# Kernel optimization log

Hardware: AMD Instinct MI355X
Metric: run time of the kernel (lower is better)

## Reference

```python
import jax, jax.numpy as jnp
import numpy as np

B, D, L = 32768, 1024, 4

def setup_inputs() -> dict:
    key = jax.random.key(0)
    k1, k2, k3 = jax.random.split(key, 3)
    x = jax.random.normal(k1, (B, D), dtype=jnp.float32)
    # torch init: normal_(0, 0.005) for both weights and biases, shape (d,1) -> flatten to (d,)
    weights = jax.random.normal(k2, (L, D), dtype=jnp.float32) * 0.005
    biases = jax.random.normal(k3, (L, D), dtype=jnp.float32) * 0.005
    return {"x": x, "weights": weights, "biases": biases}

def reference(x, weights, biases):
    # DCN cross layer: x_{i+1} = x0 * (x_i . w_i) + b_i + x_i
    # Algebraically identical to matmul(bmm(x0, x_i^T), w_i) + b_i + x_i
    x0 = x  # [B, D]

    def step(cur, wb):
        w, b = wb  # [D], [D]
        s = cur @ w  # [B] scalar per row (x_i^T w_i)
        cur = x0 * s[:, None] + b[None, :] + cur  # [B, D]
        return cur, None

    out, _ = jax.lax.scan(step, x, (weights, biases))
    return out  # [B, D] (squeeze of [B, D, 1])
```

## Files before the change

### kernel.cpp

```cpp
#include <hip/hip_runtime.h>


#define DCN_D 1024
#define DCN_F4 (DCN_D / 4)


__global__ __launch_bounds__(256) void dcn_pre_kernel(
    const float* __restrict__ w,
    const float* __restrict__ b,
    float* __restrict__ ws)
{
    const int t = threadIdx.x;
    for (int d = t; d < DCN_D; d += 256)
        ws[d] = b[d] + b[DCN_D + d] + b[2 * DCN_D + d] + b[3 * DCN_D + d];
    float p[6] = {0, 0, 0, 0, 0, 0};
    for (int d = t; d < DCN_D; d += 256) {
        const float b0 = b[d], b1 = b[DCN_D + d], b2 = b[2 * DCN_D + d];
        const float w1 = w[DCN_D + d], w2 = w[2 * DCN_D + d], w3 = w[3 * DCN_D + d];
        p[0] = fmaf(b0, w1, p[0]);
        p[1] = fmaf(b0, w2, p[1]);
        p[2] = fmaf(b1, w2, p[2]);
        p[3] = fmaf(b0, w3, p[3]);
        p[4] = fmaf(b1, w3, p[4]);
        p[5] = fmaf(b2, w3, p[5]);
    }
    __shared__ float red[6][4];
    const int wave = t >> 6, lane = t & 63;
    #pragma unroll
    for (int k = 0; k < 6; ++k) {
        float v = p[k];
        #pragma unroll
        for (int off = 32; off > 0; off >>= 1) v += __shfl_down(v, off, 64);
        if (lane == 0) red[k][wave] = v;
    }
    __syncthreads();
    if (t < 6) ws[DCN_D + t] = red[t][0] + red[t][1] + red[t][2] + red[t][3];
}

__device__ __forceinline__ void dcn_pair(
    const float4 xa[4], const float4 xb[4],
    const float4* __restrict__ w4, const float4 bv[4],
    float c01, float c2sum, float c3sum,
    float* __restrict__ out, int rowA, int rowB, int lane)
{
    float p0[4] = {0, 0, 0, 0}, p1[4] = {0, 0, 0, 0};
    #pragma unroll
    for (int j = 0; j < 4; ++j) {
        const int idx = lane + 64 * j;
        #pragma unroll
        for (int l = 0; l < 4; ++l) {
            const float4 wv = w4[l * DCN_F4 + idx];
            p0[l] = fmaf(xa[j].x, wv.x, fmaf(xa[j].y, wv.y,
                    fmaf(xa[j].z, wv.z, fmaf(xa[j].w, wv.w, p0[l]))));
            p1[l] = fmaf(xb[j].x, wv.x, fmaf(xb[j].y, wv.y,
                    fmaf(xb[j].z, wv.z, fmaf(xb[j].w, wv.w, p1[l]))));
        }
    }
    #pragma unroll
    for (int off = 1; off < 64; off <<= 1) {
        #pragma unroll
        for (int l = 0; l < 4; ++l) {
            p0[l] += __shfl_xor(p0[l], off, 64);
            p1[l] += __shfl_xor(p1[l], off, 64);
        }
    }
    const float t1a = 1.f + p0[0];
    const float s1a = fmaf(p0[1], t1a, c01);
    const float t2a = t1a + s1a;
    const float s2a = fmaf(p0[2], t2a, c2sum);
    const float t3a = t2a + s2a;
    const float s3a = fmaf(p0[3], t3a, c3sum);
    const float S0  = t3a + s3a;
    const float t1b = 1.f + p1[0];
    const float s1b = fmaf(p1[1], t1b, c01);
    const float t2b = t1b + s1b;
    const float s2b = fmaf(p1[2], t2b, c2sum);
    const float t3b = t2b + s2b;
    const float s3b = fmaf(p1[3], t3b, c3sum);
    const float S1  = t3b + s3b;

    float4* __restrict__ oA = reinterpret_cast<float4*>(out + (size_t)rowA * DCN_D);
    float4* __restrict__ oB = reinterpret_cast<float4*>(out + (size_t)rowB * DCN_D);
    #pragma unroll
    for (int j = 0; j < 4; ++j) {
        const int idx = lane + 64 * j;
        float4 a;
        a.x = fmaf(xa[j].x, S0, bv[j].x);
        a.y = fmaf(xa[j].y, S0, bv[j].y);
        a.z = fmaf(xa[j].z, S0, bv[j].z);
        a.w = fmaf(xa[j].w, S0, bv[j].w);
        oA[idx] = a;
        float4 c;
        c.x = fmaf(xb[j].x, S1, bv[j].x);
        c.y = fmaf(xb[j].y, S1, bv[j].y);
        c.z = fmaf(xb[j].z, S1, bv[j].z);
        c.w = fmaf(xb[j].w, S1, bv[j].w);
        oB[idx] = c;
    }
}

__global__ __launch_bounds__(256) void dcn_main_kernel(
    const float* __restrict__ x,
    const float* __restrict__ w,
    const float* __restrict__ ws,
    float* __restrict__ out,
    int B)
{
    const int wid  = (int)((blockIdx.x * 256u + threadIdx.x) >> 6);
    const int lane = (int)(threadIdx.x & 63);
    const int row0 = wid * 4;
    if (row0 >= B) return;

    const float4* __restrict__ w4  = reinterpret_cast<const float4*>(w);
    const float4* __restrict__ bs4 = reinterpret_cast<const float4*>(ws);

    float4 bv[4];
    #pragma unroll
    for (int j = 0; j < 4; ++j) bv[j] = bs4[lane + 64 * j];
    const float c01   = ws[DCN_D + 0];
    const float c2sum = ws[DCN_D + 1] + ws[DCN_D + 2];
    const float c3sum = ws[DCN_D + 3] + ws[DCN_D + 4] + ws[DCN_D + 5];

    float4 xv[4][4];
    #pragma unroll
    for (int r = 0; r < 4; ++r) {
        const float4* __restrict__ xr =
            reinterpret_cast<const float4*>(x + (size_t)(row0 + r) * DCN_D);
        #pragma unroll
        for (int j = 0; j < 4; ++j) xv[r][j] = xr[lane + 64 * j];
    }

    dcn_pair(xv[0], xv[1], w4, bv, c01, c2sum, c3sum, out, row0 + 0, row0 + 1, lane);
    dcn_pair(xv[2], xv[3], w4, bv, c01, c2sum, c3sum, out, row0 + 2, row0 + 3, lane);
}

extern "C" void kernel_launch(void* const* d_in, const int* in_sizes, int n_in,
                              void* d_out, int out_size, void* d_ws, size_t ws_size,
                              hipStream_t stream) {
    const float* x = (const float*)d_in[0];
    const float* w = (const float*)d_in[1];
    const float* b = (const float*)d_in[2];
    float* out = (float*)d_out;
    float* ws = (float*)d_ws;
    const int B = in_sizes[0] / DCN_D;

    dcn_pre_kernel<<<1, 256, 0, stream>>>(w, b, ws);
    const int rows_per_block = 16;
    dcn_main_kernel<<<(B + rows_per_block - 1) / rows_per_block, 256, 0, stream>>>(
        x, w, ws, out, B);
}
```

Before: 52.59 us.

## Fuse bias precompute into main kernel and process two rows per wave

Removes the separate single-block precompute kernel. Each wave now computes the summed bias and the bias-weight cross terms redundantly from L2-resident weights, then processes two rows instead of four. This drops one kernel launch and the serialized tiny pre-kernel from the timed path. In exchange every wave re-reads bias and weight vectors and does an extra reduction, and twice as many blocks are launched.

```diff
diff --git a/kernel.cpp b/kernel.cpp
--- a/kernel.cpp
+++ b/kernel.cpp
@@ -4,45 +4,64 @@
 #define DCN_D 1024
 #define DCN_F4 (DCN_D / 4)
 
+__device__ __forceinline__ float dot4acc(const float4 a, const float4 b, float acc) {
+    return fmaf(a.x, b.x, fmaf(a.y, b.y, fmaf(a.z, b.z, fmaf(a.w, b.w, acc))));
+}
 
-__global__ __launch_bounds__(256) void dcn_pre_kernel(
+__global__ __launch_bounds__(256) void dcn_fused_kernel(
+    const float* __restrict__ x,
     const float* __restrict__ w,
     const float* __restrict__ b,
-    float* __restrict__ ws)
+    float* __restrict__ out,
+    int B)
 {
-    const int t = threadIdx.x;
-    for (int d = t; d < DCN_D; d += 256)
-        ws[d] = b[d] + b[DCN_D + d] + b[2 * DCN_D + d] + b[3 * DCN_D + d];
-    float p[6] = {0, 0, 0, 0, 0, 0};
-    for (int d = t; d < DCN_D; d += 256) {
-        const float b0 = b[d], b1 = b[DCN_D + d], b2 = b[2 * DCN_D + d];
-        const float w1 = w[DCN_D + d], w2 = w[2 * DCN_D + d], w3 = w[3 * DCN_D + d];
-        p[0] = fmaf(b0, w1, p[0]);
-        p[1] = fmaf(b0, w2, p[1]);
-        p[2] = fmaf(b1, w2, p[2]);
-        p[3] = fmaf(b0, w3, p[3]);
-        p[4] = fmaf(b1, w3, p[4]);
-        p[5] = fmaf(b2, w3, p[5]);
+    const int wid  = (int)((blockIdx.x * 256u + threadIdx.x) >> 6);
+    const int lane = (int)(threadIdx.x & 63);
+    const int row0 = wid * 2;
+    if (row0 >= B) return;
+
+    const float4* __restrict__ w4 = reinterpret_cast<const float4*>(w);
+    const float4* __restrict__ b4 = reinterpret_cast<const float4*>(b);
+
+    float4 bv[4];
+    float cp0 = 0.f, cp1 = 0.f, cp2 = 0.f;
+    #pragma unroll
+    for (int j = 0; j < 4; ++j) {
+        const int idx = lane + 64 * j;
+        const float4 b0 = b4[idx];
+        const float4 b1 = b4[DCN_F4 + idx];
+        const float4 b2 = b4[2 * DCN_F4 + idx];
+        const float4 b3 = b4[3 * DCN_F4 + idx];
+        const float4 w1 = w4[DCN_F4 + idx];
+        const float4 w2 = w4[2 * DCN_F4 + idx];
+        const float4 w3 = w4[3 * DCN_F4 + idx];
+        float4 q2, q3, q4;
+        q2.x = b0.x + b1.x; q2.y = b0.y + b1.y; q2.z = b0.z + b1.z; q2.w = b0.w + b1.w;
+        q3.x = q2.x + b2.x; q3.y = q2.y + b2.y; q3.z = q2.z + b2.z; q3.w = q2.w + b2.w;
+        q4.x = q3.x + b3.x; q4.y = q3.y + b3.y; q4.z = q3.z + b3.z; q4.w = q3.w + b3.w;
+        bv[j] = q4;
+        cp0 = dot4acc(b0, w1, cp0);
+        cp1 = dot4acc(q2, w2, cp1);
+        cp2 = dot4acc(q3, w3, cp2);
     }
-    __shared__ float red[6][4];
-    const int wave = t >> 6, lane = t & 63;
+
+    const float4* __restrict__ xr0 =
+        reinterpret_cast<const float4*>(x + (size_t)row0 * DCN_D);
+    const float4* __restrict__ xr1 =
+        reinterpret_cast<const float4*>(x + (size_t)(row0 + 1) * DCN_D);
+    float4 xa[4], xb[4];
     #pragma unroll
-    for (int k = 0; k < 6; ++k) {
-        float v = p[k];
-        #pragma unroll
-        for (int off = 32; off > 0; off >>= 1) v += __shfl_down(v, off, 64);
-        if (lane == 0) red[k][wave] = v;
+    for (int j = 0; j < 4; ++j) xa[j] = xr0[lane + 64 * j];
+    #pragma unroll
+    for (int j = 0; j < 4; ++j) xb[j] = xr1[lane + 64 * j];
+
+    #pragma unroll
+    for (int off = 1; off < 64; off <<= 1) {
+        cp0 += __shfl_xor(cp0, off, 64);
+        cp1 += __shfl_xor(cp1, off, 64);
+        cp2 += __shfl_xor(cp2, off, 64);
     }
-    __syncthreads();
-    if (t < 6) ws[DCN_D + t] = red[t][0] + red[t][1] + red[t][2] + red[t][3];
-}
 
-__device__ __forceinline__ void dcn_pair(
-    const float4 xa[4], const float4 xb[4],
-    const float4* __restrict__ w4, const float4 bv[4],
-    float c01, float c2sum, float c3sum,
-    float* __restrict__ out, int rowA, int rowB, int lane)
-{
     float p0[4] = {0, 0, 0, 0}, p1[4] = {0, 0, 0, 0};
     #pragma unroll
     for (int j = 0; j < 4; ++j) {
@@ -50,10 +69,8 @@
         #pragma unroll
         for (int l = 0; l < 4; ++l) {
             const float4 wv = w4[l * DCN_F4 + idx];
-            p0[l] = fmaf(xa[j].x, wv.x, fmaf(xa[j].y, wv.y,
-                    fmaf(xa[j].z, wv.z, fmaf(xa[j].w, wv.w, p0[l]))));
-            p1[l] = fmaf(xb[j].x, wv.x, fmaf(xb[j].y, wv.y,
-                    fmaf(xb[j].z, wv.z, fmaf(xb[j].w, wv.w, p1[l]))));
+            p0[l] = dot4acc(xa[j], wv, p0[l]);
+            p1[l] = dot4acc(xb[j], wv, p1[l]);
         }
     }
     #pragma unroll
@@ -64,23 +81,24 @@
             p1[l] += __shfl_xor(p1[l], off, 64);
         }
     }
+
     const float t1a = 1.f + p0[0];
-    const float s1a = fmaf(p0[1], t1a, c01);
+    const float s1a = fmaf(p0[1], t1a, cp0);
     const float t2a = t1a + s1a;
-    const float s2a = fmaf(p0[2], t2a, c2sum);
+    const float s2a = fmaf(p0[2], t2a, cp1);
     const float t3a = t2a + s2a;
-    const float s3a = fmaf(p0[3], t3a, c3sum);
+    const float s3a = fmaf(p0[3], t3a, cp2);
     const float S0  = t3a + s3a;
     const float t1b = 1.f + p1[0];
-    const float s1b = fmaf(p1[1], t1b, c01);
+    const float s1b = fmaf(p1[1], t1b, cp0);
     const float t2b = t1b + s1b;
-    const float s2b = fmaf(p1[2], t2b, c2sum);
+    const float s2b = fmaf(p1[2], t2b, cp1);
     const float t3b = t2b + s2b;
-    const float s3b = fmaf(p1[3], t3b, c3sum);
+    const float s3b = fmaf(p1[3], t3b, cp2);
     const float S1  = t3b + s3b;
 
-    float4* __restrict__ oA = reinterpret_cast<float4*>(out + (size_t)rowA * DCN_D);
-    float4* __restrict__ oB = reinterpret_cast<float4*>(out + (size_t)rowB * DCN_D);
+    float4* __restrict__ o0 = reinterpret_cast<float4*>(out + (size_t)row0 * DCN_D);
+    float4* __restrict__ o1 = reinterpret_cast<float4*>(out + (size_t)(row0 + 1) * DCN_D);
     #pragma unroll
     for (int j = 0; j < 4; ++j) {
         const int idx = lane + 64 * j;
@@ -89,49 +107,14 @@
         a.y = fmaf(xa[j].y, S0, bv[j].y);
         a.z = fmaf(xa[j].z, S0, bv[j].z);
         a.w = fmaf(xa[j].w, S0, bv[j].w);
-        oA[idx] = a;
+        o0[idx] = a;
         float4 c;
         c.x = fmaf(xb[j].x, S1, bv[j].x);
         c.y = fmaf(xb[j].y, S1, bv[j].y);
         c.z = fmaf(xb[j].z, S1, bv[j].z);
         c.w = fmaf(xb[j].w, S1, bv[j].w);
-        oB[idx] = c;
+        o1[idx] = c;
     }
-}
-
-__global__ __launch_bounds__(256) void dcn_main_kernel(
-    const float* __restrict__ x,
-    const float* __restrict__ w,
-    const float* __restrict__ ws,
-    float* __restrict__ out,
-    int B)
-{
-    const int wid  = (int)((blockIdx.x * 256u + threadIdx.x) >> 6);
-    const int lane = (int)(threadIdx.x & 63);
-    const int row0 = wid * 4;
-    if (row0 >= B) return;
-
-    const float4* __restrict__ w4  = reinterpret_cast<const float4*>(w);
-    const float4* __restrict__ bs4 = reinterpret_cast<const float4*>(ws);
-
-    float4 bv[4];
-    #pragma unroll
-    for (int j = 0; j < 4; ++j) bv[j] = bs4[lane + 64 * j];
-    const float c01   = ws[DCN_D + 0];
-    const float c2sum = ws[DCN_D + 1] + ws[DCN_D + 2];
-    const float c3sum = ws[DCN_D + 3] + ws[DCN_D + 4] + ws[DCN_D + 5];
-
-    float4 xv[4][4];
-    #pragma unroll
-    for (int r = 0; r < 4; ++r) {
-        const float4* __restrict__ xr =
-            reinterpret_cast<const float4*>(x + (size_t)(row0 + r) * DCN_D);
-        #pragma unroll
-        for (int j = 0; j < 4; ++j) xv[r][j] = xr[lane + 64 * j];
-    }
-
-    dcn_pair(xv[0], xv[1], w4, bv, c01, c2sum, c3sum, out, row0 + 0, row0 + 1, lane);
-    dcn_pair(xv[2], xv[3], w4, bv, c01, c2sum, c3sum, out, row0 + 2, row0 + 3, lane);
 }
 
 extern "C" void kernel_launch(void* const* d_in, const int* in_sizes, int n_in,
@@ -141,11 +124,9 @@
     const float* w = (const float*)d_in[1];
     const float* b = (const float*)d_in[2];
     float* out = (float*)d_out;
-    float* ws = (float*)d_ws;
     const int B = in_sizes[0] / DCN_D;
 
-    dcn_pre_kernel<<<1, 256, 0, stream>>>(w, b, ws);
-    const int rows_per_block = 16;
-    dcn_main_kernel<<<(B + rows_per_block - 1) / rows_per_block, 256, 0, stream>>>(
-        x, w, ws, out, B);
+    const int rows_per_block = 8;
+    dcn_fused_kernel<<<(B + rows_per_block - 1) / rows_per_block, 256, 0, stream>>>(
+        x, w, b, out, B);
 }
```

Result: slower. 66.83 us (+27.1%).

## Stage weights and bias in LDS and process two rows per wave

Applied to the files above, without the earlier changes.

Each block now cooperatively loads the four weight vectors and the summed bias into shared memory, and each wave handles two rows instead of four. Weight reads in the dot-product loop come from LDS rather than global/L1, and fewer live registers (two rows of x instead of four) should allow more waves per CU to hide memory latency. In exchange there are twice as many blocks, each reloading 16 KB of weights into LDS plus a barrier, and LDS usage per block may limit occupancy.

```diff
diff --git a/kernel.cpp b/kernel.cpp
--- a/kernel.cpp
+++ b/kernel.cpp
@@ -37,25 +37,63 @@
     if (t < 6) ws[DCN_D + t] = red[t][0] + red[t][1] + red[t][2] + red[t][3];
 }
 
-__device__ __forceinline__ void dcn_pair(
-    const float4 xa[4], const float4 xb[4],
-    const float4* __restrict__ w4, const float4 bv[4],
-    float c01, float c2sum, float c3sum,
-    float* __restrict__ out, int rowA, int rowB, int lane)
+__device__ __forceinline__ float dot4acc(const float4 a, const float4 b, float acc) {
+    return fmaf(a.x, b.x, fmaf(a.y, b.y, fmaf(a.z, b.z, fmaf(a.w, b.w, acc))));
+}
+
+__global__ __launch_bounds__(256) void dcn_main_kernel(
+    const float* __restrict__ x,
+    const float* __restrict__ w,
+    const float* __restrict__ ws,
+    float* __restrict__ out,
+    int B)
 {
+    __shared__ float4 w_lds[4 * DCN_F4];
+    __shared__ float4 b_lds[DCN_F4];
+
+    const int t    = (int)threadIdx.x;
+    const int lane = t & 63;
+    const int wib  = t >> 6;
+    const int row0 = ((int)blockIdx.x * 4 + wib) * 2;
+    const bool live = row0 < B;
+    const bool has2 = (row0 + 1) < B;
+
+    float4 xa[4], xb[4];
+    if (live) {
+        const float4* __restrict__ xr0 =
+            reinterpret_cast<const float4*>(x + (size_t)row0 * DCN_D);
+        const float4* __restrict__ xr1 =
+            reinterpret_cast<const float4*>(x + (size_t)(has2 ? row0 + 1 : row0) * DCN_D);
+        #pragma unroll
+        for (int j = 0; j < 4; ++j) xa[j] = xr0[lane + 64 * j];
+        #pragma unroll
+        for (int j = 0; j < 4; ++j) xb[j] = xr1[lane + 64 * j];
+    }
+
+    const float4* __restrict__ w4  = reinterpret_cast<const float4*>(w);
+    const float4* __restrict__ bs4 = reinterpret_cast<const float4*>(ws);
+    #pragma unroll
+    for (int i = 0; i < 4; ++i) w_lds[t + 256 * i] = w4[t + 256 * i];
+    b_lds[t] = bs4[t];
+    const float c01   = ws[DCN_D + 0];
+    const float c2sum = ws[DCN_D + 1] + ws[DCN_D + 2];
+    const float c3sum = ws[DCN_D + 3] + ws[DCN_D + 4] + ws[DCN_D + 5];
+    __syncthreads();
+
+    if (!live) return;
+
     float p0[4] = {0, 0, 0, 0}, p1[4] = {0, 0, 0, 0};
     #pragma unroll
     for (int j = 0; j < 4; ++j) {
         const int idx = lane + 64 * j;
         #pragma unroll
         for (int l = 0; l < 4; ++l) {
-            const float4 wv = w4[l * DCN_F4 + idx];
-            p0[l] = fmaf(xa[j].x, wv.x, fmaf(xa[j].y, wv.y,
-                    fmaf(xa[j].z, wv.z, fmaf(xa[j].w, wv.w, p0[l]))));
-            p1[l] = fmaf(xb[j].x, wv.x, fmaf(xb[j].y, wv.y,
-                    fmaf(xb[j].z, wv.z, fmaf(xb[j].w, wv.w, p1[l]))));
+            const float4 wv = w_lds[l * DCN_F4 + idx];
+            p0[l] = dot4acc(xa[j], wv, p0[l]);
+            p1[l] = dot4acc(xb[j], wv, p1[l]);
         }
     }
+
     #pragma unroll
     for (int off = 1; off < 64; off <<= 1) {
         #pragma unroll
@@ -64,6 +102,7 @@
             p1[l] += __shfl_xor(p1[l], off, 64);
         }
     }
+
     const float t1a = 1.f + p0[0];
     const float s1a = fmaf(p0[1], t1a, c01);
     const float t2a = t1a + s1a;
@@ -79,59 +118,27 @@
     const float s3b = fmaf(p1[3], t3b, c3sum);
     const float S1  = t3b + s3b;
 
-    float4* __restrict__ oA = reinterpret_cast<float4*>(out + (size_t)rowA * DCN_D);
-    float4* __restrict__ oB = reinterpret_cast<float4*>(out + (size_t)rowB * DCN_D);
+    float4* __restrict__ o0 = reinterpret_cast<float4*>(out + (size_t)row0 * DCN_D);
+    float4* __restrict__ o1 = reinterpret_cast<float4*>(out + (size_t)(row0 + 1) * DCN_D);
     #pragma unroll
     for (int j = 0; j < 4; ++j) {
         const int idx = lane + 64 * j;
+        const float4 bb = b_lds[idx];
         float4 a;
-        a.x = fmaf(xa[j].x, S0, bv[j].x);
-        a.y = fmaf(xa[j].y, S0, bv[j].y);
-        a.z = fmaf(xa[j].z, S0, bv[j].z);
-        a.w = fmaf(xa[j].w, S0, bv[j].w);
-        oA[idx] = a;
-        float4 c;
-        c.x = fmaf(xb[j].x, S1, bv[j].x);
-        c.y = fmaf(xb[j].y, S1, bv[j].y);
-        c.z = fmaf(xb[j].z, S1, bv[j].z);
-        c.w = fmaf(xb[j].w, S1, bv[j].w);
-        oB[idx] = c;
+        a.x = fmaf(xa[j].x, S0, bb.x);
+        a.y = fmaf(xa[j].y, S0, bb.y);
+        a.z = fmaf(xa[j].z, S0, bb.z);
+        a.w = fmaf(xa[j].w, S0, bb.w);
+        o0[idx] = a;
+        if (has2) {
+            float4 c;
+            c.x = fmaf(xb[j].x, S1, bb.x);
+            c.y = fmaf(xb[j].y, S1, bb.y);
+            c.z = fmaf(xb[j].z, S1, bb.z);
+            c.w = fmaf(xb[j].w, S1, bb.w);
+            o1[idx] = c;
+        }
     }
-}
-
-__global__ __launch_bounds__(256) void dcn_main_kernel(
-    const float* __restrict__ x,
-    const float* __restrict__ w,
-    const float* __restrict__ ws,
-    float* __restrict__ out,
-    int B)
-{
-    const int wid  = (int)((blockIdx.x * 256u + threadIdx.x) >> 6);
-    const int lane = (int)(threadIdx.x & 63);
-    const int row0 = wid * 4;
-    if (row0 >= B) return;
-
-    const float4* __restrict__ w4  = reinterpret_cast<const float4*>(w);
-    const float4* __restrict__ bs4 = reinterpret_cast<const float4*>(ws);
-
-    float4 bv[4];
-    #pragma unroll
-    for (int j = 0; j < 4; ++j) bv[j] = bs4[lane + 64 * j];
-    const float c01   = ws[DCN_D + 0];
-    const float c2sum = ws[DCN_D + 1] + ws[DCN_D + 2];
-    const float c3sum = ws[DCN_D + 3] + ws[DCN_D + 4] + ws[DCN_D + 5];
-
-    float4 xv[4][4];
-    #pragma unroll
-    for (int r = 0; r < 4; ++r) {
-        const float4* __restrict__ xr =
-            reinterpret_cast<const float4*>(x + (size_t)(row0 + r) * DCN_D);
-        #pragma unroll
-        for (int j = 0; j < 4; ++j) xv[r][j] = xr[lane + 64 * j];
-    }
-
-    dcn_pair(xv[0], xv[1], w4, bv, c01, c2sum, c3sum, out, row0 + 0, row0 + 1, lane);
-    dcn_pair(xv[2], xv[3], w4, bv, c01, c2sum, c3sum, out, row0 + 2, row0 + 3, lane);
 }
 
 extern "C" void kernel_launch(void* const* d_in, const int* in_sizes, int n_in,
@@ -145,7 +152,7 @@
     const int B = in_sizes[0] / DCN_D;
 
     dcn_pre_kernel<<<1, 256, 0, stream>>>(w, b, ws);
-    const int rows_per_block = 16;
+    const int rows_per_block = 8;
     dcn_main_kernel<<<(B + rows_per_block - 1) / rows_per_block, 256, 0, stream>>>(
         x, w, ws, out, B);
 }
```

Result: faster. 50.43 us (-4.1%).
